# Kernel tuning notes

Measured on AMD Instinct MI355X. Metric: run time of the kernel, lower is better.

Reference implementation:

```python
import jax, jax.numpy as jnp
import numpy as np

N = 20000   # nodes
E = 320000  # edges (avg degree 16)
F = 8       # n_original_features (tokens per node)
D = 16      # embed_dim
H = 4       # num_heads
OUT = 7     # classes


def setup_inputs() -> dict:
    key = jax.random.key(0)
    ks = jax.random.split(key, 12)
    s = 0.1
    return {
        "x": jax.random.normal(ks[0], (N, F * D), dtype=jnp.float32),
        "edge_index": jax.random.randint(ks[1], (2, E), 0, N, dtype=jnp.int32),
        "conv1_wqkv": jax.random.normal(ks[2], (3 * D, D), dtype=jnp.float32) * s,
        "conv1_bqkv": jnp.zeros((3 * D,), dtype=jnp.float32),
        "conv1_wo": jax.random.normal(ks[3], (D, D), dtype=jnp.float32) * s,
        "conv1_bo": jnp.zeros((D,), dtype=jnp.float32),
        "conv2_wqkv": jax.random.normal(ks[4], (3 * D, D), dtype=jnp.float32) * s,
        "conv2_bqkv": jnp.zeros((3 * D,), dtype=jnp.float32),
        "conv2_wo": jax.random.normal(ks[5], (D, D), dtype=jnp.float32) * s,
        "conv2_bo": jnp.zeros((D,), dtype=jnp.float32),
        "out_w": jax.random.normal(ks[6], (OUT, F * D), dtype=jnp.float32) * s,
        "out_b": jnp.zeros((OUT,), dtype=jnp.float32),
    }


def _mha_edge(xq, xkv, wqkv, bqkv, wo, bo):
    # xq, xkv: [E, F, D]. torch MultiheadAttention: query=xq, key=value=xkv.
    dh = D // H
    wq, wk, wv = jnp.split(wqkv, 3, axis=0)
    bq, bk, bv = jnp.split(bqkv, 3)
    q = (xq @ wq.T + bq).reshape(-1, F, H, dh)
    k = (xkv @ wk.T + bk).reshape(-1, F, H, dh)
    v = (xkv @ wv.T + bv).reshape(-1, F, H, dh)
    scale = 1.0 / np.sqrt(dh).astype(np.float32)
    scores = jnp.einsum('efhd,eghd->ehfg', q, k) * scale  # [E,H,F,F]
    attn = jax.nn.softmax(scores, axis=-1)
    out = jnp.einsum('ehfg,eghd->efhd', attn, v).reshape(-1, F, D)
    return out @ wo.T + bo


def _amp_conv(x, src, dst, wqkv, bqkv, wo, bo):
    # gather per-edge token views; query = target node tokens (x_i), key/value = source (x_j)
    xj = x[src].reshape(-1, F, D)
    xi = x[dst].reshape(-1, F, D)
    msg = _mha_edge(xi, xj, wqkv, bqkv, wo, bo).reshape(-1, F * D)
    return jax.ops.segment_sum(msg, dst, num_segments=N)  # aggr='add' at targets


def reference(x, edge_index, conv1_wqkv, conv1_bqkv, conv1_wo, conv1_bo,
              conv2_wqkv, conv2_bqkv, conv2_wo, conv2_bo, out_w, out_b):
    src, dst = edge_index[0], edge_index[1]
    h = _amp_conv(x, src, dst, conv1_wqkv, conv1_bqkv, conv1_wo, conv1_bo)
    h = jax.nn.elu(h)
    h = _amp_conv(h, src, dst, conv2_wqkv, conv2_bqkv, conv2_wo, conv2_bo)
    h = jax.nn.elu(h)
    logits = h @ out_w.T + out_b
    return jax.nn.log_softmax(logits, axis=1)
```

## Files before the change

kernel.cpp:

```cpp
#include <hip/hip_runtime.h>
#include <hip/hip_bf16.h>
#include <math.h>

#define NN 20000
#define NE 320000
#define FT 8
#define DM 16
#define FD 128
#define OUTC 7
#define NFD (NN * FD)

typedef unsigned short ushort;
typedef unsigned int uint;
typedef __fp16 h2 __attribute__((ext_vector_type(2)));
union UH { uint u; h2 h; };

__device__ inline h2 u2h(uint x) { UH c; c.u = x; return c.h; }

__device__ inline float dot2(uint a, h2 b, float c) {
#if __has_builtin(__builtin_amdgcn_fdot2)
    return __builtin_amdgcn_fdot2(u2h(a), b, c, false);
#else
    h2 ah = u2h(a);
    return fmaf((float)ah.x, (float)b.x, fmaf((float)ah.y, (float)b.y, c));
#endif
}
__device__ inline float dot2u(uint a, uint b, float c) { return dot2(a, u2h(b), c); }

__device__ inline h2 pk(float a, float b) {
#if __has_builtin(__builtin_amdgcn_cvt_pkrtz)
    return __builtin_amdgcn_cvt_pkrtz(a, b);
#else
    h2 r; r.x = (__fp16)a; r.y = (__fp16)b; return r;
#endif
}
__device__ inline ushort f16b(float x) {
    union { __fp16 h; ushort u; } c; c.h = (__fp16)x; return c.u;
}
__device__ inline float rcpf(float x) {
#if __has_builtin(__builtin_amdgcn_rcpf)
    return __builtin_amdgcn_rcpf(x);
#else
    return 1.0f / x;
#endif
}

#define QSCALE 0.7213475204444817f


__global__ __launch_bounds__(256) void qkv1_kernel(
    const float* __restrict__ x,
    const float* __restrict__ wqkv, const float* __restrict__ bqkv,
    ushort* __restrict__ qout, ushort* __restrict__ kvout) {
    __shared__ float sw[48 * 17];
    __shared__ float sb[48];
    __shared__ float sx[2][FD];
    __shared__ uint squ[2][64];
    __shared__ uint skvu[2][128];
    const int t = threadIdx.x;
    const int nh = t >> 7, tl = t & 127;
    const int n = blockIdx.x * 2 + nh;
    for (int i = t; i < 48 * 16; i += 256) sw[(i >> 4) * 17 + (i & 15)] = wqkv[i];
    if (t < 48) sb[t] = bqkv[t];
    sx[nh][tl] = x[(size_t)n * FD + tl];
    __syncthreads();
    const int f = tl >> 4, d = tl & 15, h = d >> 2, dd = d & 3;
    float aq = sb[d], ak = sb[16 + d], av = sb[32 + d];
    const float* xr = &sx[nh][f * 16];
#pragma unroll
    for (int e = 0; e < 16; ++e) {
        const float xe = xr[e];
        aq = fmaf(xe, sw[d * 17 + e], aq);
        ak = fmaf(xe, sw[(16 + d) * 17 + e], ak);
        av = fmaf(xe, sw[(32 + d) * 17 + e], av);
    }
    ushort* sq = (ushort*)squ[nh];
    ushort* skv = (ushort*)skvu[nh];
    sq[tl] = f16b(aq * QSCALE);
    skv[h * 64 + f * 4 + dd] = f16b(ak);
    skv[h * 64 + 32 + dd * 8 + f] = f16b(av);
    __syncthreads();
    if (tl < 64) ((uint*)(qout + (size_t)n * FD))[tl] = squ[nh][tl];
    ((uint*)(kvout + (size_t)n * 256))[tl] = skvu[nh][tl];
}

__global__ __launch_bounds__(256) void deg_kernel(const int* __restrict__ dst,
                                                  int* __restrict__ deg) {
    const int e = blockIdx.x * 256 + threadIdx.x;
    if (e < NE) atomicAdd(&deg[dst[e]], 1);
}

__global__ __launch_bounds__(1024) void scan_kernel(const int* __restrict__ deg,
                                                    int* __restrict__ rowstart,
                                                    int* __restrict__ cursor) {
    __shared__ int wsum[16];
    __shared__ int s_carry;
    const int t = threadIdx.x;
    const int lane = t & 63, wid = t >> 6;
    if (t == 0) s_carry = 0;
    __syncthreads();
    for (int base = 0; base < NN; base += 1024) {
        const int i = base + t;
        const int d = (i < NN) ? deg[i] : 0;
        int s = d;
        for (int off = 1; off < 64; off <<= 1) {
            int tmp = __shfl_up(s, off);
            if (lane >= off) s += tmp;
        }
        if (lane == 63) wsum[wid] = s;
        __syncthreads();
        if (wid == 0) {
            int ws = (lane < 16) ? wsum[lane] : 0;
            for (int off = 1; off < 16; off <<= 1) {
                int tmp = __shfl_up(ws, off);
                if (lane >= off) ws += tmp;
            }
            if (lane < 16) wsum[lane] = ws;
        }
        __syncthreads();
        const int carry = s_carry;
        const int woff = (wid > 0) ? wsum[wid - 1] : 0;
        if (i < NN) {
            const int excl = carry + woff + s - d;
            rowstart[i] = excl;
            cursor[i] = excl;
        }
        __syncthreads();
        if (t == 1023) s_carry = carry + wsum[15];
        __syncthreads();
    }
    if (t == 0) rowstart[NN] = NE;
}

__global__ __launch_bounds__(256) void scatter_kernel(
    const int* __restrict__ src, const int* __restrict__ dst,
    int* __restrict__ cursor, int* __restrict__ csr_src) {
    const int e = blockIdx.x * 256 + threadIdx.x;
    if (e < NE) {
        const int pos = atomicAdd(&cursor[dst[e]], 1);
        csr_src[pos] = src[e];
    }
}

__global__ __launch_bounds__(256) void edge_agg_kernel(
    const int* __restrict__ rowstart, const int* __restrict__ csr_src,
    const ushort* __restrict__ qh, const uint* __restrict__ kvw,
    float* __restrict__ accum) {
    __shared__ float lred[2][FD];
    const int t = threadIdx.x;
    const int nh = t >> 7;
    const int wv = (t >> 6) & 1;
    const int w = blockIdx.x * 2 + nh;
    const int lane = t & 63;
    const int slot = lane >> 3;
    const int sub  = lane & 7;
    const int h    = sub >> 1;
    const int fh   = sub & 1;

    const uint* qrow = (const uint*)(qh + (size_t)w * FD);
    uint2 qp[4];
#pragma unroll
    for (int fi = 0; fi < 4; ++fi)
        qp[fi] = *(const uint2*)(qrow + (fh * 4 + fi) * 8 + h * 2);

    const int beg = rowstart[w], end = rowstart[w + 1];

    float acc[4][4];
#pragma unroll
    for (int fi = 0; fi < 4; ++fi)
#pragma unroll
        for (int dd = 0; dd < 4; ++dd) acc[fi][dd] = 0.f;

    int e = beg + wv * 8 + slot;
    uint idx = (e < end) ? (uint)csr_src[e] : 0u;
    float gate = (e < end) ? 1.0f : 0.0f;

    for (int eb = beg + wv * 8; eb < end; eb += 16) {
        const uint4* p = (const uint4*)(kvw + (size_t)idx * 128 + h * 32);
        const uint4 k0 = p[0], k1 = p[1], k2 = p[2], k3 = p[3];
        const uint4 v0 = p[4], v1 = p[5], v2 = p[6], v3 = p[7];
        const int en = eb + 16 + slot;
        const uint idxn = (en < end) ? (uint)csr_src[en] : 0u;
        const float gaten = (en < end) ? 1.0f : 0.0f;

#pragma unroll
        for (int fi = 0; fi < 4; ++fi) {
            const uint qx = qp[fi].x, qy = qp[fi].y;
            float s0 = dot2u(qy, k0.y, dot2u(qx, k0.x, 0.f));
            float s1 = dot2u(qy, k0.w, dot2u(qx, k0.z, 0.f));
            float s2 = dot2u(qy, k1.y, dot2u(qx, k1.x, 0.f));
            float s3 = dot2u(qy, k1.w, dot2u(qx, k1.z, 0.f));
            float s4 = dot2u(qy, k2.y, dot2u(qx, k2.x, 0.f));
            float s5 = dot2u(qy, k2.w, dot2u(qx, k2.z, 0.f));
            float s6 = dot2u(qy, k3.y, dot2u(qx, k3.x, 0.f));
            float s7 = dot2u(qy, k3.w, dot2u(qx, k3.z, 0.f));
            s0 = exp2f(s0); s1 = exp2f(s1); s2 = exp2f(s2); s3 = exp2f(s3);
            s4 = exp2f(s4); s5 = exp2f(s5); s6 = exp2f(s6); s7 = exp2f(s7);
            const float sum = ((s0 + s1) + (s2 + s3)) + ((s4 + s5) + (s6 + s7));
            const float inv = gate * rcpf(sum);
            const h2 e0 = pk(s0, s1), e1 = pk(s2, s3), e2 = pk(s4, s5), e3 = pk(s6, s7);
            const float p0 = dot2(v0.w, e3, dot2(v0.z, e2, dot2(v0.y, e1, dot2(v0.x, e0, 0.f))));
            const float p1 = dot2(v1.w, e3, dot2(v1.z, e2, dot2(v1.y, e1, dot2(v1.x, e0, 0.f))));
            const float p2 = dot2(v2.w, e3, dot2(v2.z, e2, dot2(v2.y, e1, dot2(v2.x, e0, 0.f))));
            const float p3 = dot2(v3.w, e3, dot2(v3.z, e2, dot2(v3.y, e1, dot2(v3.x, e0, 0.f))));
            acc[fi][0] = fmaf(p0, inv, acc[fi][0]);
            acc[fi][1] = fmaf(p1, inv, acc[fi][1]);
            acc[fi][2] = fmaf(p2, inv, acc[fi][2]);
            acc[fi][3] = fmaf(p3, inv, acc[fi][3]);
        }
        idx = idxn; gate = gaten;
    }

#pragma unroll
    for (int fi = 0; fi < 4; ++fi)
#pragma unroll
        for (int dd = 0; dd < 4; ++dd) {
            float a = acc[fi][dd];
            a += __shfl_xor(a, 8);
            a += __shfl_xor(a, 16);
            a += __shfl_xor(a, 32);
            acc[fi][dd] = a;
        }
    if (wv == 1 && slot == 0) {
#pragma unroll
        for (int fi = 0; fi < 4; ++fi) {
            const int f = fh * 4 + fi;
            *(float4*)(&lred[nh][f * 16 + h * 4]) =
                make_float4(acc[fi][0], acc[fi][1], acc[fi][2], acc[fi][3]);
        }
    }
    __syncthreads();
    if (wv == 0 && slot == 0) {
        float* arow = accum + (size_t)w * FD;
#pragma unroll
        for (int fi = 0; fi < 4; ++fi) {
            const int f = fh * 4 + fi;
            const float4 o = *(const float4*)(&lred[nh][f * 16 + h * 4]);
            *(float4*)(arow + f * 16 + h * 4) =
                make_float4(acc[fi][0] + o.x, acc[fi][1] + o.y,
                            acc[fi][2] + o.z, acc[fi][3] + o.w);
        }
    }
}

__global__ __launch_bounds__(256) void post_qkv_kernel(
    const float* __restrict__ accum, const int* __restrict__ deg,
    const float* __restrict__ wo, const float* __restrict__ bo,
    const float* __restrict__ wqkv, const float* __restrict__ bqkv,
    ushort* __restrict__ qout, ushort* __restrict__ kvout) {
    __shared__ float swo[16 * 17];
    __shared__ float sbo[16];
    __shared__ float swq[48 * 17];
    __shared__ float sbq[48];
    __shared__ float sa[2][FD];
    __shared__ float sh[2][FD];
    __shared__ uint squ[2][64];
    __shared__ uint skvu[2][128];
    const int t = threadIdx.x;
    const int nh = t >> 7, tl = t & 127;
    const int n = blockIdx.x * 2 + nh;
    for (int i = t; i < 16 * 16; i += 256) swo[(i >> 4) * 17 + (i & 15)] = wo[i];
    for (int i = t; i < 48 * 16; i += 256) swq[(i >> 4) * 17 + (i & 15)] = wqkv[i];
    if (t < 16) sbo[t] = bo[t];
    if (t < 48) sbq[t] = bqkv[t];
    sa[nh][tl] = accum[(size_t)n * FD + tl];
    __syncthreads();
    const int f = tl >> 4, d = tl & 15, h = d >> 2, dd = d & 3;
    float hv = (float)deg[n] * sbo[d];
#pragma unroll
    for (int e = 0; e < 16; ++e) hv = fmaf(sa[nh][f * 16 + e], swo[d * 17 + e], hv);
    hv = hv > 0.f ? hv : expm1f(hv);
    sh[nh][tl] = hv;
    __syncthreads();
    float aq = sbq[d], ak = sbq[16 + d], av = sbq[32 + d];
    const float* xr = &sh[nh][f * 16];
#pragma unroll
    for (int e = 0; e < 16; ++e) {
        const float xe = xr[e];
        aq = fmaf(xe, swq[d * 17 + e], aq);
        ak = fmaf(xe, swq[(16 + d) * 17 + e], ak);
        av = fmaf(xe, swq[(32 + d) * 17 + e], av);
    }
    ushort* sq = (ushort*)squ[nh];
    ushort* skv = (ushort*)skvu[nh];
    sq[tl] = f16b(aq * QSCALE);
    skv[h * 64 + f * 4 + dd] = f16b(ak);
    skv[h * 64 + 32 + dd * 8 + f] = f16b(av);
    __syncthreads();
    if (tl < 64) ((uint*)(qout + (size_t)n * FD))[tl] = squ[nh][tl];
    ((uint*)(kvout + (size_t)n * 256))[tl] = skvu[nh][tl];
}

__global__ __launch_bounds__(256) void post_cls_kernel(
    const float* __restrict__ accum, const int* __restrict__ deg,
    const float* __restrict__ wo, const float* __restrict__ bo,
    const float* __restrict__ cw, const float* __restrict__ cb,
    float* __restrict__ out) {
    __shared__ float swo[16 * 17];
    __shared__ float sbo[16];
    __shared__ float scw[OUTC * FD];
    __shared__ float sa[2][FD];
    __shared__ float sred[2][2][OUTC];
    const int t = threadIdx.x;
    const int nh = t >> 7, tl = t & 127;
    const int n = blockIdx.x * 2 + nh;
    for (int i = t; i < 16 * 16; i += 256) swo[(i >> 4) * 17 + (i & 15)] = wo[i];
    for (int i = t; i < OUTC * FD; i += 256) scw[i] = cw[i];
    if (t < 16) sbo[t] = bo[t];
    sa[nh][tl] = accum[(size_t)n * FD + tl];
    __syncthreads();
    const int f = tl >> 4, d = tl & 15;
    const int lane = t & 63, wid = (t >> 6) & 1;
    float hv = (float)deg[n] * sbo[d];
#pragma unroll
    for (int e = 0; e < 16; ++e) hv = fmaf(sa[nh][f * 16 + e], swo[d * 17 + e], hv);
    hv = hv > 0.f ? hv : expm1f(hv);
    float p[OUTC];
#pragma unroll
    for (int c = 0; c < OUTC; ++c) p[c] = hv * scw[c * FD + tl];
#pragma unroll
    for (int c = 0; c < OUTC; ++c)
        for (int off = 32; off; off >>= 1) p[c] += __shfl_xor(p[c], off);
    if (lane == 0)
#pragma unroll
        for (int c = 0; c < OUTC; ++c) sred[nh][wid][c] = p[c];
    __syncthreads();
    if (tl == 0) {
        float lg[OUTC];
        float m = -1e30f;
#pragma unroll
        for (int c = 0; c < OUTC; ++c) {
            lg[c] = sred[nh][0][c] + sred[nh][1][c] + cb[c];
            m = fmaxf(m, lg[c]);
        }
        float s = 0.f;
#pragma unroll
        for (int c = 0; c < OUTC; ++c) s += __expf(lg[c] - m);
        const float lse = m + logf(s);
#pragma unroll
        for (int c = 0; c < OUTC; ++c) out[(size_t)n * OUTC + c] = lg[c] - lse;
    }
}

extern "C" void kernel_launch(void* const* d_in, const int* in_sizes, int n_in,
                              void* d_out, int out_size, void* d_ws, size_t ws_size,
                              hipStream_t stream) {
    const float* x      = (const float*)d_in[0];
    const int*   ei     = (const int*)d_in[1];
    const float* w1qkv  = (const float*)d_in[2];
    const float* b1qkv  = (const float*)d_in[3];
    const float* w1o    = (const float*)d_in[4];
    const float* b1o    = (const float*)d_in[5];
    const float* w2qkv  = (const float*)d_in[6];
    const float* b2qkv  = (const float*)d_in[7];
    const float* w2o    = (const float*)d_in[8];
    const float* b2o    = (const float*)d_in[9];
    const float* outw   = (const float*)d_in[10];
    const float* outb   = (const float*)d_in[11];
    float* out = (float*)d_out;

    const int* srcp = ei;
    const int* dstp = ei + NE;

    ushort* qh    = (ushort*)d_ws;
    ushort* kvh   = qh + (size_t)NN * FD;
    float*  accum = (float*)(kvh + (size_t)NN * 256);
    int*    deg      = (int*)(accum + NFD);
    int*    rowstart = deg + NN;
    int*    cursor   = rowstart + NN + 1;
    int*    csr_src  = cursor + NN;

    (void)hipMemsetAsync(deg, 0, NN * sizeof(int), stream);
    deg_kernel<<<(NE + 255) / 256, 256, 0, stream>>>(dstp, deg);
    scan_kernel<<<1, 1024, 0, stream>>>(deg, rowstart, cursor);
    scatter_kernel<<<(NE + 255) / 256, 256, 0, stream>>>(srcp, dstp, cursor, csr_src);

    qkv1_kernel<<<NN / 2, 256, 0, stream>>>(x, w1qkv, b1qkv, qh, kvh);
    edge_agg_kernel<<<NN / 2, 256, 0, stream>>>(rowstart, csr_src, qh, (const uint*)kvh, accum);
    post_qkv_kernel<<<NN / 2, 256, 0, stream>>>(accum, deg, w1o, b1o, w2qkv, b2qkv, qh, kvh);
    edge_agg_kernel<<<NN / 2, 256, 0, stream>>>(rowstart, csr_src, qh, (const uint*)kvh, accum);
    post_cls_kernel<<<NN / 2, 256, 0, stream>>>(accum, deg, w2o, b2o, outw, outb, out);
}
```

Baseline: 236.1 us.

## Map one wavefront per node in edge aggregation and use raw exp2

The edge aggregation kernel now gives each node a single 64-lane wavefront (16 edge slots by 4 heads) instead of two wavefronts that each split the query tokens in half. Each lane now covers all 8 query tokens, so the LDS cross-wave reduction and __syncthreads are gone, and the launch grid is halved. Each edge's K/V row is loaded once rather than twice, at the cost of twice the accumulator registers and a longer unrolled inner loop, which may reduce occupancy. exp2f is also swapped for the raw hardware exp2 builtin.

```diff
diff --git a/kernel.cpp b/kernel.cpp
--- a/kernel.cpp
+++ b/kernel.cpp
@@ -42,6 +42,13 @@
     return __builtin_amdgcn_rcpf(x);
 #else
     return 1.0f / x;
+#endif
+}
+__device__ inline float exp2r(float x) {
+#if __has_builtin(__builtin_amdgcn_exp2f)
+    return __builtin_amdgcn_exp2f(x);
+#else
+    return exp2f(x);
 #endif
 }
 
@@ -146,36 +153,31 @@
     const int* __restrict__ rowstart, const int* __restrict__ csr_src,
     const ushort* __restrict__ qh, const uint* __restrict__ kvw,
     float* __restrict__ accum) {
-    __shared__ float lred[2][FD];
-    const int t = threadIdx.x;
-    const int nh = t >> 7;
-    const int wv = (t >> 6) & 1;
-    const int w = blockIdx.x * 2 + nh;
-    const int lane = t & 63;
-    const int slot = lane >> 3;
-    const int sub  = lane & 7;
-    const int h    = sub >> 1;
-    const int fh   = sub & 1;
+    const int w = (blockIdx.x * 256 + threadIdx.x) >> 6;
+    if (w >= NN) return;
+    const int lane = threadIdx.x & 63;
+    const int slot = lane >> 2;
+    const int h    = lane & 3;
 
     const uint* qrow = (const uint*)(qh + (size_t)w * FD);
-    uint2 qp[4];
-#pragma unroll
-    for (int fi = 0; fi < 4; ++fi)
-        qp[fi] = *(const uint2*)(qrow + (fh * 4 + fi) * 8 + h * 2);
+    uint2 qp[8];
+#pragma unroll
+    for (int f = 0; f < 8; ++f)
+        qp[f] = *(const uint2*)(qrow + f * 8 + h * 2);
 
     const int beg = rowstart[w], end = rowstart[w + 1];
 
-    float acc[4][4];
-#pragma unroll
-    for (int fi = 0; fi < 4; ++fi)
-#pragma unroll
-        for (int dd = 0; dd < 4; ++dd) acc[fi][dd] = 0.f;
-
-    int e = beg + wv * 8 + slot;
+    float acc[8][4];
+#pragma unroll
+    for (int f = 0; f < 8; ++f)
+#pragma unroll
+        for (int dd = 0; dd < 4; ++dd) acc[f][dd] = 0.f;
+
+    int e = beg + slot;
     uint idx = (e < end) ? (uint)csr_src[e] : 0u;
     float gate = (e < end) ? 1.0f : 0.0f;
 
-    for (int eb = beg + wv * 8; eb < end; eb += 16) {
+    for (int eb = beg; eb < end; eb += 16) {
         const uint4* p = (const uint4*)(kvw + (size_t)idx * 128 + h * 32);
         const uint4 k0 = p[0], k1 = p[1], k2 = p[2], k3 = p[3];
         const uint4 v0 = p[4], v1 = p[5], v2 = p[6], v3 = p[7];
@@ -184,8 +186,8 @@
         const float gaten = (en < end) ? 1.0f : 0.0f;
 
 #pragma unroll
-        for (int fi = 0; fi < 4; ++fi) {
-            const uint qx = qp[fi].x, qy = qp[fi].y;
+        for (int f = 0; f < 8; ++f) {
+            const uint qx = qp[f].x, qy = qp[f].y;
             float s0 = dot2u(qy, k0.y, dot2u(qx, k0.x, 0.f));
             float s1 = dot2u(qy, k0.w, dot2u(qx, k0.z, 0.f));
             float s2 = dot2u(qy, k1.y, dot2u(qx, k1.x, 0.f));
@@ -194,8 +196,8 @@
             float s5 = dot2u(qy, k2.w, dot2u(qx, k2.z, 0.f));
             float s6 = dot2u(qy, k3.y, dot2u(qx, k3.x, 0.f));
             float s7 = dot2u(qy, k3.w, dot2u(qx, k3.z, 0.f));
-            s0 = exp2f(s0); s1 = exp2f(s1); s2 = exp2f(s2); s3 = exp2f(s3);
-            s4 = exp2f(s4); s5 = exp2f(s5); s6 = exp2f(s6); s7 = exp2f(s7);
+            s0 = exp2r(s0); s1 = exp2r(s1); s2 = exp2r(s2); s3 = exp2r(s3);
+            s4 = exp2r(s4); s5 = exp2r(s5); s6 = exp2r(s6); s7 = exp2r(s7);
             const float sum = ((s0 + s1) + (s2 + s3)) + ((s4 + s5) + (s6 + s7));
             const float inv = gate * rcpf(sum);
             const h2 e0 = pk(s0, s1), e1 = pk(s2, s3), e2 = pk(s4, s5), e3 = pk(s6, s7);
@@ -203,43 +205,31 @@
             const float p1 = dot2(v1.w, e3, dot2(v1.z, e2, dot2(v1.y, e1, dot2(v1.x, e0, 0.f))));
             const float p2 = dot2(v2.w, e3, dot2(v2.z, e2, dot2(v2.y, e1, dot2(v2.x, e0, 0.f))));
             const float p3 = dot2(v3.w, e3, dot2(v3.z, e2, dot2(v3.y, e1, dot2(v3.x, e0, 0.f))));
-            acc[fi][0] = fmaf(p0, inv, acc[fi][0]);
-            acc[fi][1] = fmaf(p1, inv, acc[fi][1]);
-            acc[fi][2] = fmaf(p2, inv, acc[fi][2]);
-            acc[fi][3] = fmaf(p3, inv, acc[fi][3]);
+            acc[f][0] = fmaf(p0, inv, acc[f][0]);
+            acc[f][1] = fmaf(p1, inv, acc[f][1]);
+            acc[f][2] = fmaf(p2, inv, acc[f][2]);
+            acc[f][3] = fmaf(p3, inv, acc[f][3]);
         }
         idx = idxn; gate = gaten;
     }
 
 #pragma unroll
-    for (int fi = 0; fi < 4; ++fi)
+    for (int f = 0; f < 8; ++f)
 #pragma unroll
         for (int dd = 0; dd < 4; ++dd) {
-            float a = acc[fi][dd];
+            float a = acc[f][dd];
+            a += __shfl_xor(a, 4);
             a += __shfl_xor(a, 8);
             a += __shfl_xor(a, 16);
             a += __shfl_xor(a, 32);
-            acc[fi][dd] = a;
-        }
-    if (wv == 1 && slot == 0) {
-#pragma unroll
-        for (int fi = 0; fi < 4; ++fi) {
-            const int f = fh * 4 + fi;
-            *(float4*)(&lred[nh][f * 16 + h * 4]) =
-                make_float4(acc[fi][0], acc[fi][1], acc[fi][2], acc[fi][3]);
-        }
-    }
-    __syncthreads();
-    if (wv == 0 && slot == 0) {
+            acc[f][dd] = a;
+        }
+    if (slot == 0) {
         float* arow = accum + (size_t)w * FD;
 #pragma unroll
-        for (int fi = 0; fi < 4; ++fi) {
-            const int f = fh * 4 + fi;
-            const float4 o = *(const float4*)(&lred[nh][f * 16 + h * 4]);
+        for (int f = 0; f < 8; ++f)
             *(float4*)(arow + f * 16 + h * 4) =
-                make_float4(acc[fi][0] + o.x, acc[fi][1] + o.y,
-                            acc[fi][2] + o.z, acc[fi][3] + o.w);
-        }
+                make_float4(acc[f][0], acc[f][1], acc[f][2], acc[f][3]);
     }
 }
 
@@ -376,8 +366,8 @@
     scatter_kernel<<<(NE + 255) / 256, 256, 0, stream>>>(srcp, dstp, cursor, csr_src);
 
     qkv1_kernel<<<NN / 2, 256, 0, stream>>>(x, w1qkv, b1qkv, qh, kvh);
-    edge_agg_kernel<<<NN / 2, 256, 0, stream>>>(rowstart, csr_src, qh, (const uint*)kvh, accum);
+    edge_agg_kernel<<<NN / 4, 256, 0, stream>>>(rowstart, csr_src, qh, (const uint*)kvh, accum);
     post_qkv_kernel<<<NN / 2, 256, 0, stream>>>(accum, deg, w1o, b1o, w2qkv, b2qkv, qh, kvh);
-    edge_agg_kernel<<<NN / 2, 256, 0, stream>>>(rowstart, csr_src, qh, (const uint*)kvh, accum);
+    edge_agg_kernel<<<NN / 4, 256, 0, stream>>>(rowstart, csr_src, qh, (const uint*)kvh, accum);
     post_cls_kernel<<<NN / 2, 256, 0, stream>>>(accum, deg, w2o, b2o, outw, outb, out);
 }
```

New measurement: 228.4 us. -3.3%, faster.
